# Kernel optimization log

Hardware: AMD Instinct MI355X
Metric: run time of the kernel (lower is better)

## Reference

```python
import jax, jax.numpy as jnp
import numpy as np
import math

E = 1024   # embedding_dim
H = 16     # num_attention_heads
DH = 64    # head_embedding_dim
THD = H * DH
EPS = 1e-5

def _layernorm(x, g, b):
    m = jnp.mean(x, axis=-1, keepdims=True)
    v = jnp.mean(jnp.square(x - m), axis=-1, keepdims=True)
    return (x - m) * jax.lax.rsqrt(v + EPS) * g + b

def setup_inputs() -> dict:
    key = jax.random.key(0)
    ks = jax.random.split(key, 16)
    s_in = 1.0 / math.sqrt(E)
    s_o = 1.0 / math.sqrt(THD)
    inp = {"tokens": jax.random.normal(ks[0], (2, 2048, E), dtype=jnp.float32)}
    # q_linear / k_linear / v_linear: LayerNorm(E) then Linear(E -> THD)
    for i, name in enumerate(["q", "k", "v"]):
        inp[f"ln_{name}_g"] = jnp.ones((E,), jnp.float32)
        inp[f"ln_{name}_b"] = jnp.zeros((E,), jnp.float32)
        inp[f"W{name}"] = jax.random.uniform(ks[1 + 2 * i], (E, THD), jnp.float32, -s_in, s_in)
        inp[f"b{name}"] = jax.random.uniform(ks[2 + 2 * i], (THD,), jnp.float32, -s_in, s_in)
    # attention_linear: LayerNorm(THD) then Linear(THD -> E)
    inp["ln_o_g"] = jnp.ones((THD,), jnp.float32)
    inp["ln_o_b"] = jnp.zeros((THD,), jnp.float32)
    inp["Wo"] = jax.random.uniform(ks[7], (THD, E), jnp.float32, -s_o, s_o)
    inp["bo"] = jax.random.uniform(ks[8], (E,), jnp.float32, -s_o, s_o)
    return inp

def reference(tokens, ln_q_g, ln_q_b, Wq, bq, ln_k_g, ln_k_b, Wk, bk,
              ln_v_g, ln_v_b, Wv, bv, ln_o_g, ln_o_b, Wo, bo):
    N, L, _ = tokens.shape
    # NOTE: faithful to source quirk -- k comes from v_linear, v comes from k_linear.
    q = (_layernorm(tokens, ln_q_g, ln_q_b) @ Wq + bq).reshape(N, L, H, DH).transpose(0, 2, 1, 3)  # (N,H,L,Dh)
    k = (_layernorm(tokens, ln_v_g, ln_v_b) @ Wv + bv).reshape(N, L, H, DH).transpose(0, 2, 3, 1)  # (N,H,Dh,L)
    v = (_layernorm(tokens, ln_k_g, ln_k_b) @ Wk + bk).reshape(N, L, H, DH).transpose(0, 2, 1, 3)  # (N,H,L,Dh)
    qkT = jnp.einsum('bhid,bhdj->bhij', q, k)  # (N,H,L,L)
    # mask added BEFORE dividing by sqrt(Dh), as in source
    mask = jnp.triu(jnp.full((L, L), -9999.0, dtype=qkT.dtype), k=1)
    attn = jax.nn.softmax((qkT + mask) / math.sqrt(DH), axis=-1)
    wv = jnp.einsum('bhij,bhjd->bhid', attn, v).transpose(0, 2, 1, 3).reshape(N, L, THD)
    out = _layernorm(wv, ln_o_g, ln_o_b) @ Wo + bo + tokens
    return (out, k, v)
```

## Files before the change

kernel.cpp:

```cpp
#include <hip/hip_runtime.h>

#define L_SEQ 2048
#define NH    16
#define E_DIM 1024
#define M_ROWS 4096

typedef unsigned short u16;
typedef unsigned int   u32;
typedef __attribute__((ext_vector_type(8))) __bf16 bf16x8;
typedef __attribute__((ext_vector_type(4))) float  f32x4;

__device__ __forceinline__ u16 f2bf(float f) {
  union { float f; u32 u; } x; x.f = f;
  u32 u = x.u;
  return (u16)((u + 0x7FFFu + ((u >> 16) & 1u)) >> 16);
}
__device__ __forceinline__ float bf2f(u16 v) {
  union { u32 u; float f; } x; x.u = ((u32)v) << 16;
  return x.f;
}
__device__ __forceinline__ void st_bf4(u16* p, float a, float b, float c, float d) {
  ushort4 u; u.x = f2bf(a); u.y = f2bf(b); u.z = f2bf(c); u.w = f2bf(d);
  *reinterpret_cast<ushort4*>(p) = u;
}
__device__ __forceinline__ void gload16(const u16* g, u16* l) {
  __builtin_amdgcn_global_load_lds(
      (const __attribute__((address_space(1))) void*)g,
      (__attribute__((address_space(3))) void*)l, 16, 0, 0);
}
#define SBAR() asm volatile("s_barrier" ::: "memory")

__global__ __launch_bounds__(256) void ln_hat_f32(const float* __restrict__ x, u16* __restrict__ o)
{
  __shared__ float red[8];
  const size_t row = blockIdx.x;
  const int t = threadIdx.x;
  float4 v = reinterpret_cast<const float4*>(x + row * E_DIM)[t];
  float s = v.x + v.y + v.z + v.w;
  float q = v.x*v.x + v.y*v.y + v.z*v.z + v.w*v.w;
  #pragma unroll
  for (int off = 32; off; off >>= 1) { s += __shfl_down(s, off); q += __shfl_down(q, off); }
  if ((t & 63) == 0) { red[t >> 6] = s; red[4 + (t >> 6)] = q; }
  __syncthreads();
  float S = red[0] + red[1] + red[2] + red[3];
  float Q = red[4] + red[5] + red[6] + red[7];
  float mean = S * (1.f / E_DIM);
  float rstd = rsqrtf(Q * (1.f / E_DIM) - mean * mean + 1e-5f);
  st_bf4(o + row * E_DIM + t * 4,
         (v.x - mean) * rstd, (v.y - mean) * rstd, (v.z - mean) * rstd, (v.w - mean) * rstd);
}

__global__ __launch_bounds__(256) void ln_hat_bf16(const u16* __restrict__ x, u16* __restrict__ o)
{
  __shared__ float red[8];
  const size_t row = blockIdx.x;
  const int t = threadIdx.x;
  ushort4 u = reinterpret_cast<const ushort4*>(x + row * E_DIM)[t];
  float v0 = bf2f(u.x), v1 = bf2f(u.y), v2 = bf2f(u.z), v3 = bf2f(u.w);
  float s = v0 + v1 + v2 + v3;
  float q = v0*v0 + v1*v1 + v2*v2 + v3*v3;
  #pragma unroll
  for (int off = 32; off; off >>= 1) { s += __shfl_down(s, off); q += __shfl_down(q, off); }
  if ((t & 63) == 0) { red[t >> 6] = s; red[4 + (t >> 6)] = q; }
  __syncthreads();
  float S = red[0] + red[1] + red[2] + red[3];
  float Q = red[4] + red[5] + red[6] + red[7];
  float mean = S * (1.f / E_DIM);
  float rstd = rsqrtf(Q * (1.f / E_DIM) - mean * mean + 1e-5f);
  st_bf4(o + row * E_DIM + t * 4,
         (v0 - mean) * rstd, (v1 - mean) * rstd, (v2 - mean) * rstd, (v3 - mean) * rstd);
}

__global__ __launch_bounds__(256) void transpose_all(
    const float* __restrict__ W0, const float* __restrict__ W1,
    const float* __restrict__ W2, const float* __restrict__ W3,
    const float* __restrict__ g0, const float* __restrict__ g1,
    const float* __restrict__ g2, const float* __restrict__ g3,
    u16* __restrict__ T0, u16* __restrict__ T1, u16* __restrict__ T2, u16* __restrict__ T3)
{
  __shared__ float tile[32][33];
  const int z = blockIdx.z;
  const float* W = (z == 0) ? W0 : (z == 1) ? W1 : (z == 2) ? W2 : W3;
  const float* g = (z == 0) ? g0 : (z == 1) ? g1 : (z == 2) ? g2 : g3;
  u16* T = (z == 0) ? T0 : (z == 1) ? T1 : (z == 2) ? T2 : T3;
  const int tx = threadIdx.x & 31, ty = threadIdx.x >> 5;
  const int bx = blockIdx.x * 32, by = blockIdx.y * 32;
  #pragma unroll
  for (int r = 0; r < 4; ++r) {
    const int e = by + ty + r * 8;
    tile[ty + r * 8][tx] = W[(size_t)e * E_DIM + bx + tx] * g[e];
  }
  __syncthreads();
  #pragma unroll
  for (int r = 0; r < 4; ++r)
    T[(size_t)(bx + ty + r * 8) * E_DIM + by + tx] = f2bf(tile[tx][ty + r * 8]);
}

__global__ __launch_bounds__(256) void bias_fold(
    const float* __restrict__ W0, const float* __restrict__ W1,
    const float* __restrict__ W2, const float* __restrict__ W3,
    const float* __restrict__ l0, const float* __restrict__ l1,
    const float* __restrict__ l2, const float* __restrict__ l3,
    const float* __restrict__ b0, const float* __restrict__ b1,
    const float* __restrict__ b2, const float* __restrict__ b3,
    float* __restrict__ bfold)
{
  __shared__ float part[8][32];
  const int z = blockIdx.y;
  const float* W  = (z == 0) ? W0 : (z == 1) ? W1 : (z == 2) ? W2 : W3;
  const float* bl = (z == 0) ? l0 : (z == 1) ? l1 : (z == 2) ? l2 : l3;
  const float* bs = (z == 0) ? b0 : (z == 1) ? b1 : (z == 2) ? b2 : b3;
  const int tn = threadIdx.x & 31, te = threadIdx.x >> 5;
  const int n = blockIdx.x * 32 + tn;
  float acc = 0.f;
  const int e0 = te * 128;
  for (int e = e0; e < e0 + 128; ++e) acc += bl[e] * W[(size_t)e * E_DIM + n];
  part[te][tn] = acc;
  __syncthreads();
  if (te == 0) {
    float s = part[0][tn] + part[1][tn] + part[2][tn] + part[3][tn]
            + part[4][tn] + part[5][tn] + part[6][tn] + part[7][tn];
    bfold[z * E_DIM + n] = bs[n] + s;
  }
}

#define GBK 64
__device__ __forceinline__ void core128(
    const u16* __restrict__ A, const u16* __restrict__ BT,
    int m0, int n0, int t, u16* lds, f32x4 (&acc)[4][4])
{
  const int lane = t & 63, wave = t >> 6;
  const int wm = wave >> 1, wn = wave & 1;
  const int fr = lane & 15, hi = lane >> 4;
  const int sx = fr & 7;

  auto STAGE = [&](int buf, int kt) {
    u16* la = lds + (buf * 2 + 0) * (128 * GBK);
    u16* lb = lds + (buf * 2 + 1) * (128 * GBK);
    #pragma unroll
    for (int s = 0; s < 4; ++s) {
      const int seg = t + s * 256;
      const int r = seg >> 3;
      const int gc = (seg & 7) ^ (r & 7);
      gload16(A + (size_t)(m0 + r) * E_DIM + kt * GBK + gc * 8, la + seg * 8);
    }
    #pragma unroll
    for (int s = 0; s < 4; ++s) {
      const int seg = t + s * 256;
      const int r = seg >> 3;
      const int gc = (seg & 7) ^ (r & 7);
      gload16(BT + (size_t)(n0 + r) * E_DIM + kt * GBK + gc * 8, lb + seg * 8);
    }
  };
  auto AF = [&](int buf, int i, int ks) -> bf16x8 {
    return *reinterpret_cast<const bf16x8*>(
        lds + (buf * 2 + 0) * (128 * GBK) + (wm * 64 + i * 16 + fr) * GBK + (((ks * 4 + hi) ^ sx) * 8));
  };
  auto BF = [&](int buf, int j, int ks) -> bf16x8 {
    return *reinterpret_cast<const bf16x8*>(
        lds + (buf * 2 + 1) * (128 * GBK) + (wn * 64 + j * 16 + fr) * GBK + (((ks * 4 + hi) ^ sx) * 8));
  };
  auto PHASES = [&](int buf) {
    bf16x8 a[4][2], b[4][2];
    #pragma unroll
    for (int i = 0; i < 4; ++i) { a[i][0] = AF(buf, i, 0); a[i][1] = AF(buf, i, 1); }
    #pragma unroll
    for (int j = 0; j < 4; ++j) { b[j][0] = BF(buf, j, 0); b[j][1] = BF(buf, j, 1); }
    __builtin_amdgcn_s_setprio(1);
    #pragma unroll
    for (int i = 0; i < 4; ++i)
      #pragma unroll
      for (int j = 0; j < 4; ++j) {
        acc[i][j] = __builtin_amdgcn_mfma_f32_16x16x32_bf16(a[i][0], b[j][0], acc[i][j], 0, 0, 0);
        acc[i][j] = __builtin_amdgcn_mfma_f32_16x16x32_bf16(a[i][1], b[j][1], acc[i][j], 0, 0, 0);
      }
    __builtin_amdgcn_s_setprio(0);
  };

  STAGE(0, 0);
  #pragma unroll 1
  for (int kt = 0; kt < 15; ++kt) {
    const int buf = kt & 1;
    SBAR();
    STAGE(buf ^ 1, kt + 1);
    asm volatile("s_waitcnt vmcnt(8)" ::: "memory");
    SBAR();
    PHASES(buf);
  }
  asm volatile("s_waitcnt vmcnt(0)" ::: "memory");
  SBAR();
  PHASES(1);
}

__global__ __launch_bounds__(256, 2) void gemm_qkv128(
    const u16* __restrict__ xhat, const u16* __restrict__ WTcat,
    const float* __restrict__ bfold,
    float* __restrict__ kout, float* __restrict__ vout,
    u16* __restrict__ qbf, u16* __restrict__ kbf, u16* __restrict__ vTb)
{
  __shared__ u16 lds[4 * 128 * GBK];
  const int t = threadIdx.x;
  const int sw = (blockIdx.x & 7) * 96 + (blockIdx.x >> 3);
  const int by = sw / 24, bx = sw % 24;
  const int m0 = by * 128, n0 = bx * 128;

  f32x4 acc[4][4] = {};
  core128(xhat, WTcat, m0, n0, t, lds, acc);

  const int lane = t & 63, wave = t >> 6;
  const int wm = wave >> 1, wn = wave & 1;
  const int fr = lane & 15, hi = lane >> 4;
  const int z = n0 >> 10;
  const float* bias = bfold + z * E_DIM;
  const int rowb = hi * 4;
  #pragma unroll
  for (int i = 0; i < 4; ++i) {
    const int mbase = m0 + wm * 64 + i * 16 + rowb;
    #pragma unroll
    for (int j = 0; j < 4; ++j) {
      const int ng = n0 + wn * 64 + j * 16 + fr;
      const int ncol = ng & 1023;
      const float bval = bias[ncol];
      #pragma unroll
      for (int r = 0; r < 4; ++r) {
        const int m = mbase + r;
        const float val = acc[i][j][r] + bval;
        const int b = m >> 11, l = m & 2047, h = ncol >> 6, d = ncol & 63;
        const size_t bh = (size_t)(b * NH + h);
        if (z == 0) {
          qbf[((bh * L_SEQ + l) << 6) + d] = f2bf(val);
        } else if (z == 1) {
          kout[(bh * 64 + d) * L_SEQ + l] = val;
          kbf[((bh * L_SEQ + l) << 6) + d] = f2bf(val);
        } else {
          vout[(bh * L_SEQ + l) * 64 + d] = val;
          vTb[(bh * 64 + d) * L_SEQ + l] = f2bf(val);
        }
      }
    }
  }
}

__global__ __launch_bounds__(256, 2) void gemm_o128(
    const u16* __restrict__ A, const u16* __restrict__ BT, const float* __restrict__ bias,
    const float* __restrict__ tokens, float* __restrict__ out)
{
  __shared__ u16 lds[4 * 128 * GBK];
  const int t = threadIdx.x;
  const int sw = (blockIdx.x & 7) * 32 + (blockIdx.x >> 3);
  const int by = sw / 8, bx = sw % 8;
  const int m0 = by * 128, n0 = bx * 128;

  f32x4 acc[4][4] = {};
  core128(A, BT, m0, n0, t, lds, acc);

  const int lane = t & 63, wave = t >> 6;
  const int wm = wave >> 1, wn = wave & 1;
  const int fr = lane & 15, hi = lane >> 4;
  const int rowb = hi * 4;
  #pragma unroll
  for (int i = 0; i < 4; ++i) {
    const int mbase = m0 + wm * 64 + i * 16 + rowb;
    #pragma unroll
    for (int j = 0; j < 4; ++j) {
      const int ncol = n0 + wn * 64 + j * 16 + fr;
      const float bval = bias[ncol];
      #pragma unroll
      for (int r = 0; r < 4; ++r) {
        const int m = mbase + r;
        out[(size_t)m * E_DIM + ncol] = acc[i][j][r] + bval + tokens[(size_t)m * E_DIM + ncol];
      }
    }
  }
}

__global__ __launch_bounds__(256) void attn_mfma(
    const u16* __restrict__ qbf, const u16* __restrict__ kbf,
    const u16* __restrict__ vTb, u16* __restrict__ wv)
{
  __shared__ u16 Klds[64][72];
  __shared__ u16 Vlds[64][72];
  __shared__ u16 Plds[4][16][72];
  const int t = threadIdx.x, lane = t & 63, wave = t >> 6;
  const int bi = blockIdx.x;
  const int bh = (bi & 7) + 8 * ((bi >> 3) & 3);
  const int pr = bi >> 5;
  const int fr = lane & 15, hi = lane >> 4;
  const u16* kbase = kbf + (size_t)bh * L_SEQ * 64;
  const u16* vbase = vTb + (size_t)bh * 64 * L_SEQ;
  const int b = bh >> 4, h = bh & 15;

  #pragma unroll 1
  for (int half = 0; half < 2; ++half) {
    const int qt = half ? (31 - pr) : pr;
    const int q0w = qt * 64 + wave * 16;
    const int qg = q0w + fr;

    const u16* qrow = qbf + ((size_t)bh * L_SEQ + q0w + fr) * 64 + hi * 8;
    const bf16x8 qf0 = *reinterpret_cast<const bf16x8*>(qrow);
    const bf16x8 qf1 = *reinterpret_cast<const bf16x8*>(qrow + 32);

    f32x4 o[4] = {};
    float mrun = -3.0e38f, lrun = 0.f;

    for (int tkv = 0; tkv <= qt; ++tkv) {
      const int j0 = tkv * 64;
      const bool diag = (tkv == qt);
      #pragma unroll
      for (int s = 0; s < 2; ++s) {
        const int seg = t + s * 256;
        const int r = seg >> 3, c8 = (seg & 7) * 8;
        *reinterpret_cast<uint4*>(&Klds[r][c8]) =
            *reinterpret_cast<const uint4*>(kbase + (size_t)(j0 + r) * 64 + c8);
        *reinterpret_cast<uint4*>(&Vlds[r][c8]) =
            *reinterpret_cast<const uint4*>(vbase + (size_t)r * L_SEQ + j0 + c8);
      }
      __syncthreads();

      f32x4 st[4] = {};
      __builtin_amdgcn_s_setprio(1);
      #pragma unroll
      for (int kt = 0; kt < 4; ++kt) {
        bf16x8 ka0 = *reinterpret_cast<const bf16x8*>(&Klds[kt*16 + fr][hi*8]);
        bf16x8 ka1 = *reinterpret_cast<const bf16x8*>(&Klds[kt*16 + fr][32 + hi*8]);
        st[kt] = __builtin_amdgcn_mfma_f32_16x16x32_bf16(ka0, qf0, st[kt], 0, 0, 0);
        st[kt] = __builtin_amdgcn_mfma_f32_16x16x32_bf16(ka1, qf1, st[kt], 0, 0, 0);
      }
      __builtin_amdgcn_s_setprio(0);

      float p[16];
      float pmax = -3.0e38f;
      #pragma unroll
      for (int kt = 0; kt < 4; ++kt)
        #pragma unroll
        for (int r = 0; r < 4; ++r) {
          const int key = j0 + kt*16 + hi*4 + r;
          const float v = st[kt][r] * 0.125f +
                          ((diag && key > qg) ? -1249.875f : 0.f);
          p[kt*4 + r] = v;
          pmax = fmaxf(pmax, v);
        }
      pmax = fmaxf(pmax, __shfl_xor(pmax, 16));
      pmax = fmaxf(pmax, __shfl_xor(pmax, 32));
      const float mnew = fmaxf(mrun, pmax);
      const float alpha = __expf(mrun - mnew);
      float lsum = 0.f;
      #pragma unroll
      for (int i = 0; i < 16; ++i) { p[i] = __expf(p[i] - mnew); lsum += p[i]; }
      lsum += __shfl_xor(lsum, 16);
      lsum += __shfl_xor(lsum, 32);
      lrun = lrun * alpha + lsum;
      mrun = mnew;
      #pragma unroll
      for (int r = 0; r < 4; ++r) {
        const float ar = __shfl(alpha, hi*4 + r);
        o[0][r] *= ar; o[1][r] *= ar; o[2][r] *= ar; o[3][r] *= ar;
      }

      #pragma unroll
      for (int kt = 0; kt < 4; ++kt) {
        ushort4 w4;
        w4.x = f2bf(p[kt*4+0]); w4.y = f2bf(p[kt*4+1]);
        w4.z = f2bf(p[kt*4+2]); w4.w = f2bf(p[kt*4+3]);
        *reinterpret_cast<ushort4*>(&Plds[wave][fr][kt*16 + hi*4]) = w4;
      }

      const bf16x8 pf0 = *reinterpret_cast<const bf16x8*>(&Plds[wave][fr][hi*8]);
      const bf16x8 pf1 = *reinterpret_cast<const bf16x8*>(&Plds[wave][fr][32 + hi*8]);
      __builtin_amdgcn_s_setprio(1);
      #pragma unroll
      for (int dt = 0; dt < 4; ++dt) {
        bf16x8 vf0 = *reinterpret_cast<const bf16x8*>(&Vlds[dt*16 + fr][hi*8]);
        bf16x8 vf1 = *reinterpret_cast<const bf16x8*>(&Vlds[dt*16 + fr][32 + hi*8]);
        o[dt] = __builtin_amdgcn_mfma_f32_16x16x32_bf16(pf0, vf0, o[dt], 0, 0, 0);
        o[dt] = __builtin_amdgcn_mfma_f32_16x16x32_bf16(pf1, vf1, o[dt], 0, 0, 0);
      }
      __builtin_amdgcn_s_setprio(0);
      __syncthreads();
    }

    const float inv = 1.f / lrun;
    #pragma unroll
    for (int r = 0; r < 4; ++r) {
      const float ir = __shfl(inv, hi*4 + r);
      const int q = q0w + hi*4 + r;
      u16* dst = wv + (size_t)(b * L_SEQ + q) * E_DIM + h * 64 + fr;
      #pragma unroll
      for (int dt = 0; dt < 4; ++dt)
        dst[dt * 16] = f2bf(o[dt][r] * ir);
    }
  }
}

extern "C" void kernel_launch(void* const* d_in, const int* in_sizes, int n_in,
                              void* d_out, int out_size, void* d_ws, size_t ws_size,
                              hipStream_t stream) {
  (void)in_sizes; (void)n_in; (void)out_size; (void)ws_size;
  const float* tokens = (const float*)d_in[0];
  const float* ln_q_g = (const float*)d_in[1];
  const float* ln_q_b = (const float*)d_in[2];
  const float* Wq     = (const float*)d_in[3];
  const float* bq     = (const float*)d_in[4];
  const float* ln_k_g = (const float*)d_in[5];
  const float* ln_k_b = (const float*)d_in[6];
  const float* Wk     = (const float*)d_in[7];
  const float* bk     = (const float*)d_in[8];
  const float* ln_v_g = (const float*)d_in[9];
  const float* ln_v_b = (const float*)d_in[10];
  const float* Wv     = (const float*)d_in[11];
  const float* bv     = (const float*)d_in[12];
  const float* ln_o_g = (const float*)d_in[13];
  const float* ln_o_b = (const float*)d_in[14];
  const float* Wo     = (const float*)d_in[15];
  const float* bo     = (const float*)d_in[16];

  float* out  = (float*)d_out;
  float* kout = out + 4194304;
  float* vout = kout + 4194304;

  char* w = (char*)d_ws;
  const size_t MB = (size_t)1 << 20;
  u16*   WTq   = (u16*)(w + 0 * MB);
  u16*   WTv   = (u16*)(w + 2 * MB);
  u16*   WTk   = (u16*)(w + 4 * MB);
  u16*   WTo   = (u16*)(w + 6 * MB);
  u16*   xhat  = (u16*)(w + 8 * MB);
  u16*   qbf   = (u16*)(w + 16 * MB);
  u16*   kbf   = (u16*)(w + 24 * MB);
  u16*   vTb   = (u16*)(w + 32 * MB);
  u16*   what  = (u16*)(w + 40 * MB);
  float* bfold = (float*)(w + 48 * MB);
  u16*   wvb   = xhat;

  transpose_all<<<dim3(32, 32, 4), 256, 0, stream>>>(
      Wq, Wv, Wk, Wo, ln_q_g, ln_v_g, ln_k_g, ln_o_g, WTq, WTv, WTk, WTo);
  bias_fold<<<dim3(32, 4), 256, 0, stream>>>(
      Wq, Wv, Wk, Wo, ln_q_b, ln_v_b, ln_k_b, ln_o_b, bq, bv, bk, bo, bfold);
  ln_hat_f32<<<M_ROWS, 256, 0, stream>>>(tokens, xhat);
  gemm_qkv128<<<768, 256, 0, stream>>>(xhat, WTq, bfold, kout, vout, qbf, kbf, vTb);
  attn_mfma<<<512, 256, 0, stream>>>(qbf, kbf, vTb, wvb);
  ln_hat_bf16<<<M_ROWS, 256, 0, stream>>>(wvb, what);
  gemm_o128<<<256, 256, 0, stream>>>(what, WTo, bfold + 3 * E_DIM, tokens, out);
}
```

Before: 142.7 us.

## Shrink GEMM K-tile, double-buffer attention KV, lazy rescale, one q-tile per block

The GEMM core's K-tile drops from 64 to 32 and the XOR swizzle is removed, halving LDS per block so occupancy can rise to 3 blocks per CU. The attention kernel stages K/V for the next tile in registers and double-buffers it in LDS to overlap loads with compute. It also skips rescaling the output when the running max grows by at most 8. Each block now handles one query tile instead of a paired early/late tile, with twice the grid. Removing the swizzle may cause LDS bank conflicts, and the unpaired tiles leave blocks with unequal amounts of causal work.

```diff
diff --git a/kernel.cpp b/kernel.cpp
--- a/kernel.cpp
+++ b/kernel.cpp
@@ -124,7 +124,7 @@
   }
 }
 
-#define GBK 64
+#define GBK 32
 __device__ __forceinline__ void core128(
     const u16* __restrict__ A, const u16* __restrict__ BT,
     int m0, int n0, int t, u16* lds, f32x4 (&acc)[4][4])
@@ -132,58 +132,49 @@
   const int lane = t & 63, wave = t >> 6;
   const int wm = wave >> 1, wn = wave & 1;
   const int fr = lane & 15, hi = lane >> 4;
-  const int sx = fr & 7;
 
   auto STAGE = [&](int buf, int kt) {
     u16* la = lds + (buf * 2 + 0) * (128 * GBK);
     u16* lb = lds + (buf * 2 + 1) * (128 * GBK);
     #pragma unroll
-    for (int s = 0; s < 4; ++s) {
+    for (int s = 0; s < 2; ++s) {
       const int seg = t + s * 256;
-      const int r = seg >> 3;
-      const int gc = (seg & 7) ^ (r & 7);
-      gload16(A + (size_t)(m0 + r) * E_DIM + kt * GBK + gc * 8, la + seg * 8);
-    }
-    #pragma unroll
-    for (int s = 0; s < 4; ++s) {
+      const int r = seg >> 2, c8 = (seg & 3) * 8;
+      gload16(A + (size_t)(m0 + r) * E_DIM + kt * GBK + c8, la + seg * 8);
+    }
+    #pragma unroll
+    for (int s = 0; s < 2; ++s) {
       const int seg = t + s * 256;
-      const int r = seg >> 3;
-      const int gc = (seg & 7) ^ (r & 7);
-      gload16(BT + (size_t)(n0 + r) * E_DIM + kt * GBK + gc * 8, lb + seg * 8);
-    }
-  };
-  auto AF = [&](int buf, int i, int ks) -> bf16x8 {
-    return *reinterpret_cast<const bf16x8*>(
-        lds + (buf * 2 + 0) * (128 * GBK) + (wm * 64 + i * 16 + fr) * GBK + (((ks * 4 + hi) ^ sx) * 8));
-  };
-  auto BF = [&](int buf, int j, int ks) -> bf16x8 {
-    return *reinterpret_cast<const bf16x8*>(
-        lds + (buf * 2 + 1) * (128 * GBK) + (wn * 64 + j * 16 + fr) * GBK + (((ks * 4 + hi) ^ sx) * 8));
+      const int r = seg >> 2, c8 = (seg & 3) * 8;
+      gload16(BT + (size_t)(n0 + r) * E_DIM + kt * GBK + c8, lb + seg * 8);
+    }
   };
   auto PHASES = [&](int buf) {
-    bf16x8 a[4][2], b[4][2];
-    #pragma unroll
-    for (int i = 0; i < 4; ++i) { a[i][0] = AF(buf, i, 0); a[i][1] = AF(buf, i, 1); }
-    #pragma unroll
-    for (int j = 0; j < 4; ++j) { b[j][0] = BF(buf, j, 0); b[j][1] = BF(buf, j, 1); }
+    const u16* la = lds + (buf * 2 + 0) * (128 * GBK);
+    const u16* lb = lds + (buf * 2 + 1) * (128 * GBK);
+    bf16x8 a[4], b[4];
+    #pragma unroll
+    for (int i = 0; i < 4; ++i)
+      a[i] = *reinterpret_cast<const bf16x8*>(&la[(wm * 64 + i * 16 + fr) * GBK + hi * 8]);
+    #pragma unroll
+    for (int j = 0; j < 4; ++j)
+      b[j] = *reinterpret_cast<const bf16x8*>(&lb[(wn * 64 + j * 16 + fr) * GBK + hi * 8]);
     __builtin_amdgcn_s_setprio(1);
     #pragma unroll
     for (int i = 0; i < 4; ++i)
       #pragma unroll
-      for (int j = 0; j < 4; ++j) {
-        acc[i][j] = __builtin_amdgcn_mfma_f32_16x16x32_bf16(a[i][0], b[j][0], acc[i][j], 0, 0, 0);
-        acc[i][j] = __builtin_amdgcn_mfma_f32_16x16x32_bf16(a[i][1], b[j][1], acc[i][j], 0, 0, 0);
-      }
+      for (int j = 0; j < 4; ++j)
+        acc[i][j] = __builtin_amdgcn_mfma_f32_16x16x32_bf16(a[i], b[j], acc[i][j], 0, 0, 0);
     __builtin_amdgcn_s_setprio(0);
   };
 
   STAGE(0, 0);
   #pragma unroll 1
-  for (int kt = 0; kt < 15; ++kt) {
+  for (int kt = 0; kt < 31; ++kt) {
     const int buf = kt & 1;
     SBAR();
     STAGE(buf ^ 1, kt + 1);
-    asm volatile("s_waitcnt vmcnt(8)" ::: "memory");
+    asm volatile("s_waitcnt vmcnt(4)" ::: "memory");
     SBAR();
     PHASES(buf);
   }
@@ -192,7 +183,7 @@
   PHASES(1);
 }
 
-__global__ __launch_bounds__(256, 2) void gemm_qkv128(
+__global__ __launch_bounds__(256, 3) void gemm_qkv128(
     const u16* __restrict__ xhat, const u16* __restrict__ WTcat,
     const float* __restrict__ bfold,
     float* __restrict__ kout, float* __restrict__ vout,
@@ -241,7 +232,7 @@
   }
 }
 
-__global__ __launch_bounds__(256, 2) void gemm_o128(
+__global__ __launch_bounds__(256, 3) void gemm_o128(
     const u16* __restrict__ A, const u16* __restrict__ BT, const float* __restrict__ bias,
     const float* __restrict__ tokens, float* __restrict__ out)
 {
@@ -278,117 +269,130 @@
     const u16* __restrict__ qbf, const u16* __restrict__ kbf,
     const u16* __restrict__ vTb, u16* __restrict__ wv)
 {
-  __shared__ u16 Klds[64][72];
-  __shared__ u16 Vlds[64][72];
+  __shared__ u16 Klds[2][64][72];
+  __shared__ u16 Vlds[2][64][72];
   __shared__ u16 Plds[4][16][72];
   const int t = threadIdx.x, lane = t & 63, wave = t >> 6;
   const int bi = blockIdx.x;
   const int bh = (bi & 7) + 8 * ((bi >> 3) & 3);
-  const int pr = bi >> 5;
+  const int qt = 31 - (bi >> 5);
   const int fr = lane & 15, hi = lane >> 4;
   const u16* kbase = kbf + (size_t)bh * L_SEQ * 64;
   const u16* vbase = vTb + (size_t)bh * 64 * L_SEQ;
   const int b = bh >> 4, h = bh & 15;
 
+  const int q0w = qt * 64 + wave * 16;
+  const int qg = q0w + fr;
+  const u16* qrow = qbf + ((size_t)bh * L_SEQ + q0w + fr) * 64 + hi * 8;
+  const bf16x8 qf0 = *reinterpret_cast<const bf16x8*>(qrow);
+  const bf16x8 qf1 = *reinterpret_cast<const bf16x8*>(qrow + 32);
+
+  f32x4 o[4] = {};
+  float mrun = -3.0e38f, lrun = 0.f;
+
+  uint4 kreg[2], vreg[2];
+  auto LD = [&](int j0) {
+    #pragma unroll
+    for (int s = 0; s < 2; ++s) {
+      const int seg = t + s * 256, r = seg >> 3, c8 = (seg & 7) * 8;
+      kreg[s] = *reinterpret_cast<const uint4*>(kbase + (size_t)(j0 + r) * 64 + c8);
+      vreg[s] = *reinterpret_cast<const uint4*>(vbase + (size_t)r * L_SEQ + j0 + c8);
+    }
+  };
+  auto ST = [&](int buf) {
+    #pragma unroll
+    for (int s = 0; s < 2; ++s) {
+      const int seg = t + s * 256, r = seg >> 3, c8 = (seg & 7) * 8;
+      *reinterpret_cast<uint4*>(&Klds[buf][r][c8]) = kreg[s];
+      *reinterpret_cast<uint4*>(&Vlds[buf][r][c8]) = vreg[s];
+    }
+  };
+
+  LD(0); ST(0);
+  __syncthreads();
   #pragma unroll 1
-  for (int half = 0; half < 2; ++half) {
-    const int qt = half ? (31 - pr) : pr;
-    const int q0w = qt * 64 + wave * 16;
-    const int qg = q0w + fr;
-
-    const u16* qrow = qbf + ((size_t)bh * L_SEQ + q0w + fr) * 64 + hi * 8;
-    const bf16x8 qf0 = *reinterpret_cast<const bf16x8*>(qrow);
-    const bf16x8 qf1 = *reinterpret_cast<const bf16x8*>(qrow + 32);
-
-    f32x4 o[4] = {};
-    float mrun = -3.0e38f, lrun = 0.f;
-
-    for (int tkv = 0; tkv <= qt; ++tkv) {
-      const int j0 = tkv * 64;
-      const bool diag = (tkv == qt);
+  for (int tkv = 0; tkv <= qt; ++tkv) {
+    const int buf = tkv & 1;
+    const int j0 = tkv * 64;
+    const bool diag = (tkv == qt);
+    if (tkv < qt) LD(j0 + 64);
+
+    f32x4 st[4] = {};
+    __builtin_amdgcn_s_setprio(1);
+    #pragma unroll
+    for (int kt = 0; kt < 4; ++kt) {
+      bf16x8 ka0 = *reinterpret_cast<const bf16x8*>(&Klds[buf][kt*16 + fr][hi*8]);
+      bf16x8 ka1 = *reinterpret_cast<const bf16x8*>(&Klds[buf][kt*16 + fr][32 + hi*8]);
+      st[kt] = __builtin_amdgcn_mfma_f32_16x16x32_bf16(ka0, qf0, st[kt], 0, 0, 0);
+      st[kt] = __builtin_amdgcn_mfma_f32_16x16x32_bf16(ka1, qf1, st[kt], 0, 0, 0);
+    }
+    __builtin_amdgcn_s_setprio(0);
+
+    float p[16];
+    float pmax = -3.0e38f;
+    #pragma unroll
+    for (int kt = 0; kt < 4; ++kt)
       #pragma unroll
-      for (int s = 0; s < 2; ++s) {
-        const int seg = t + s * 256;
-        const int r = seg >> 3, c8 = (seg & 7) * 8;
-        *reinterpret_cast<uint4*>(&Klds[r][c8]) =
-            *reinterpret_cast<const uint4*>(kbase + (size_t)(j0 + r) * 64 + c8);
-        *reinterpret_cast<uint4*>(&Vlds[r][c8]) =
-            *reinterpret_cast<const uint4*>(vbase + (size_t)r * L_SEQ + j0 + c8);
+      for (int r = 0; r < 4; ++r) {
+        const int key = j0 + kt*16 + hi*4 + r;
+        const float v = st[kt][r] * 0.125f +
+                        ((diag && key > qg) ? -1249.875f : 0.f);
+        p[kt*4 + r] = v;
+        pmax = fmaxf(pmax, v);
       }
-      __syncthreads();
-
-      f32x4 st[4] = {};
-      __builtin_amdgcn_s_setprio(1);
-      #pragma unroll
-      for (int kt = 0; kt < 4; ++kt) {
-        bf16x8 ka0 = *reinterpret_cast<const bf16x8*>(&Klds[kt*16 + fr][hi*8]);
-        bf16x8 ka1 = *reinterpret_cast<const bf16x8*>(&Klds[kt*16 + fr][32 + hi*8]);
-        st[kt] = __builtin_amdgcn_mfma_f32_16x16x32_bf16(ka0, qf0, st[kt], 0, 0, 0);
-        st[kt] = __builtin_amdgcn_mfma_f32_16x16x32_bf16(ka1, qf1, st[kt], 0, 0, 0);
-      }
-      __builtin_amdgcn_s_setprio(0);
-
-      float p[16];
-      float pmax = -3.0e38f;
-      #pragma unroll
-      for (int kt = 0; kt < 4; ++kt)
-        #pragma unroll
-        for (int r = 0; r < 4; ++r) {
-          const int key = j0 + kt*16 + hi*4 + r;
-          const float v = st[kt][r] * 0.125f +
-                          ((diag && key > qg) ? -1249.875f : 0.f);
-          p[kt*4 + r] = v;
-          pmax = fmaxf(pmax, v);
-        }
-      pmax = fmaxf(pmax, __shfl_xor(pmax, 16));
-      pmax = fmaxf(pmax, __shfl_xor(pmax, 32));
+    pmax = fmaxf(pmax, __shfl_xor(pmax, 16));
+    pmax = fmaxf(pmax, __shfl_xor(pmax, 32));
+    if (!__all(pmax - mrun <= 8.f)) {
       const float mnew = fmaxf(mrun, pmax);
       const float alpha = __expf(mrun - mnew);
-      float lsum = 0.f;
-      #pragma unroll
-      for (int i = 0; i < 16; ++i) { p[i] = __expf(p[i] - mnew); lsum += p[i]; }
-      lsum += __shfl_xor(lsum, 16);
-      lsum += __shfl_xor(lsum, 32);
-      lrun = lrun * alpha + lsum;
-      mrun = mnew;
       #pragma unroll
       for (int r = 0; r < 4; ++r) {
         const float ar = __shfl(alpha, hi*4 + r);
         o[0][r] *= ar; o[1][r] *= ar; o[2][r] *= ar; o[3][r] *= ar;
       }
-
-      #pragma unroll
-      for (int kt = 0; kt < 4; ++kt) {
-        ushort4 w4;
-        w4.x = f2bf(p[kt*4+0]); w4.y = f2bf(p[kt*4+1]);
-        w4.z = f2bf(p[kt*4+2]); w4.w = f2bf(p[kt*4+3]);
-        *reinterpret_cast<ushort4*>(&Plds[wave][fr][kt*16 + hi*4]) = w4;
-      }
-
-      const bf16x8 pf0 = *reinterpret_cast<const bf16x8*>(&Plds[wave][fr][hi*8]);
-      const bf16x8 pf1 = *reinterpret_cast<const bf16x8*>(&Plds[wave][fr][32 + hi*8]);
-      __builtin_amdgcn_s_setprio(1);
-      #pragma unroll
-      for (int dt = 0; dt < 4; ++dt) {
-        bf16x8 vf0 = *reinterpret_cast<const bf16x8*>(&Vlds[dt*16 + fr][hi*8]);
-        bf16x8 vf1 = *reinterpret_cast<const bf16x8*>(&Vlds[dt*16 + fr][32 + hi*8]);
-        o[dt] = __builtin_amdgcn_mfma_f32_16x16x32_bf16(pf0, vf0, o[dt], 0, 0, 0);
-        o[dt] = __builtin_amdgcn_mfma_f32_16x16x32_bf16(pf1, vf1, o[dt], 0, 0, 0);
-      }
-      __builtin_amdgcn_s_setprio(0);
-      __syncthreads();
-    }
-
-    const float inv = 1.f / lrun;
-    #pragma unroll
-    for (int r = 0; r < 4; ++r) {
-      const float ir = __shfl(inv, hi*4 + r);
-      const int q = q0w + hi*4 + r;
-      u16* dst = wv + (size_t)(b * L_SEQ + q) * E_DIM + h * 64 + fr;
-      #pragma unroll
-      for (int dt = 0; dt < 4; ++dt)
-        dst[dt * 16] = f2bf(o[dt][r] * ir);
-    }
+      lrun *= alpha;
+      mrun = mnew;
+    }
+    float lsum = 0.f;
+    #pragma unroll
+    for (int i = 0; i < 16; ++i) { p[i] = __expf(p[i] - mrun); lsum += p[i]; }
+    lsum += __shfl_xor(lsum, 16);
+    lsum += __shfl_xor(lsum, 32);
+    lrun += lsum;
+
+    #pragma unroll
+    for (int kt = 0; kt < 4; ++kt) {
+      ushort4 w4;
+      w4.x = f2bf(p[kt*4+0]); w4.y = f2bf(p[kt*4+1]);
+      w4.z = f2bf(p[kt*4+2]); w4.w = f2bf(p[kt*4+3]);
+      *reinterpret_cast<ushort4*>(&Plds[wave][fr][kt*16 + hi*4]) = w4;
+    }
+
+    const bf16x8 pf0 = *reinterpret_cast<const bf16x8*>(&Plds[wave][fr][hi*8]);
+    const bf16x8 pf1 = *reinterpret_cast<const bf16x8*>(&Plds[wave][fr][32 + hi*8]);
+    __builtin_amdgcn_s_setprio(1);
+    #pragma unroll
+    for (int dt = 0; dt < 4; ++dt) {
+      bf16x8 vf0 = *reinterpret_cast<const bf16x8*>(&Vlds[buf][dt*16 + fr][hi*8]);
+      bf16x8 vf1 = *reinterpret_cast<const bf16x8*>(&Vlds[buf][dt*16 + fr][32 + hi*8]);
+      o[dt] = __builtin_amdgcn_mfma_f32_16x16x32_bf16(pf0, vf0, o[dt], 0, 0, 0);
+      o[dt] = __builtin_amdgcn_mfma_f32_16x16x32_bf16(pf1, vf1, o[dt], 0, 0, 0);
+    }
+    __builtin_amdgcn_s_setprio(0);
+
+    if (tkv < qt) ST(buf ^ 1);
+    __syncthreads();
+  }
+
+  const float inv = 1.f / lrun;
+  #pragma unroll
+  for (int r = 0; r < 4; ++r) {
+    const float ir = __shfl(inv, hi*4 + r);
+    const int q = q0w + hi*4 + r;
+    u16* dst = wv + (size_t)(b * L_SEQ + q) * E_DIM + h * 64 + fr;
+    #pragma unroll
+    for (int dt = 0; dt < 4; ++dt)
+      dst[dt * 16] = f2bf(o[dt][r] * ir);
   }
 }
 
@@ -438,7 +442,7 @@
       Wq, Wv, Wk, Wo, ln_q_b, ln_v_b, ln_k_b, ln_o_b, bq, bv, bk, bo, bfold);
   ln_hat_f32<<<M_ROWS, 256, 0, stream>>>(tokens, xhat);
   gemm_qkv128<<<768, 256, 0, stream>>>(xhat, WTq, bfold, kout, vout, qbf, kbf, vTb);
-  attn_mfma<<<512, 256, 0, stream>>>(qbf, kbf, vTb, wvb);
+  attn_mfma<<<1024, 256, 0, stream>>>(qbf, kbf, vTb, wvb);
   ln_hat_bf16<<<M_ROWS, 256, 0, stream>>>(wvb, what);
   gemm_o128<<<256, 256, 0, stream>>>(what, WTo, bfold + 3 * E_DIM, tokens, out);
 }
```

New measurement: 176.2 us. 1.23x slower.

## Remap GEMM tiles per XCD, use exp2 softmax and packed bf16 conversion

Applied to the files above, without the earlier changes.

Changes the block-to-tile mapping of the QKV and output GEMMs so that each XCD works on a contiguous 2D patch of tiles, which should improve L2 reuse of A and B panels. In attention, the softmax scale is folded with log2(e) so exp2f can replace __expf, and the mask constant is rescaled to match. P is converted to bf16 with the packed hip_bf16 intrinsic instead of manual per-element rounding. These are independent tweaks, and the mask constant is a rounded approximation of -1249.875·log2e.

```diff
diff --git a/kernel.cpp b/kernel.cpp
--- a/kernel.cpp
+++ b/kernel.cpp
@@ -1,4 +1,5 @@
 #include <hip/hip_runtime.h>
+#include <hip/hip_bf16.h>
 
 #define L_SEQ 2048
 #define NH    16
@@ -22,6 +23,10 @@
 __device__ __forceinline__ void st_bf4(u16* p, float a, float b, float c, float d) {
   ushort4 u; u.x = f2bf(a); u.y = f2bf(b); u.z = f2bf(c); u.w = f2bf(d);
   *reinterpret_cast<ushort4*>(p) = u;
+}
+__device__ __forceinline__ u32 pkbf(float a, float b) {
+  __hip_bfloat162 h = __float22bfloat162_rn(float2{a, b});
+  return *reinterpret_cast<u32*>(&h);
 }
 __device__ __forceinline__ void gload16(const u16* g, u16* l) {
   __builtin_amdgcn_global_load_lds(
@@ -200,8 +205,9 @@
 {
   __shared__ u16 lds[4 * 128 * GBK];
   const int t = threadIdx.x;
-  const int sw = (blockIdx.x & 7) * 96 + (blockIdx.x >> 3);
-  const int by = sw / 24, bx = sw % 24;
+  const int xcd = blockIdx.x & 7, l = blockIdx.x >> 3;
+  const int by = 8 * (xcd >> 1) + l / 12;
+  const int bx = 12 * (xcd & 1) + l % 12;
   const int m0 = by * 128, n0 = bx * 128;
 
   f32x4 acc[4][4] = {};
@@ -225,16 +231,16 @@
       for (int r = 0; r < 4; ++r) {
         const int m = mbase + r;
         const float val = acc[i][j][r] + bval;
-        const int b = m >> 11, l = m & 2047, h = ncol >> 6, d = ncol & 63;
+        const int b = m >> 11, ltok = m & 2047, h = ncol >> 6, d = ncol & 63;
         const size_t bh = (size_t)(b * NH + h);
         if (z == 0) {
-          qbf[((bh * L_SEQ + l) << 6) + d] = f2bf(val);
+          qbf[((bh * L_SEQ + ltok) << 6) + d] = f2bf(val);
         } else if (z == 1) {
-          kout[(bh * 64 + d) * L_SEQ + l] = val;
-          kbf[((bh * L_SEQ + l) << 6) + d] = f2bf(val);
+          kout[(bh * 64 + d) * L_SEQ + ltok] = val;
+          kbf[((bh * L_SEQ + ltok) << 6) + d] = f2bf(val);
         } else {
-          vout[(bh * L_SEQ + l) * 64 + d] = val;
-          vTb[(bh * 64 + d) * L_SEQ + l] = f2bf(val);
+          vout[(bh * L_SEQ + ltok) * 64 + d] = val;
+          vTb[(bh * 64 + d) * L_SEQ + ltok] = f2bf(val);
         }
       }
     }
@@ -247,8 +253,9 @@
 {
   __shared__ u16 lds[4 * 128 * GBK];
   const int t = threadIdx.x;
-  const int sw = (blockIdx.x & 7) * 32 + (blockIdx.x >> 3);
-  const int by = sw / 8, bx = sw % 8;
+  const int xcd = blockIdx.x & 7, l = blockIdx.x >> 3;
+  const int by = 8 * (xcd >> 1) + (l >> 2);
+  const int bx = 4 * (xcd & 1) + (l & 3);
   const int m0 = by * 128, n0 = bx * 128;
 
   f32x4 acc[4][4] = {};
@@ -289,6 +296,8 @@
   const u16* kbase = kbf + (size_t)bh * L_SEQ * 64;
   const u16* vbase = vTb + (size_t)bh * 64 * L_SEQ;
   const int b = bh >> 4, h = bh & 15;
+  const float kSC2  = 0.125f * 1.44269504089f;
+  const float kMSK2 = -1803.2f;
 
   #pragma unroll 1
   for (int half = 0; half < 2; ++half) {
@@ -335,18 +344,17 @@
         #pragma unroll
         for (int r = 0; r < 4; ++r) {
           const int key = j0 + kt*16 + hi*4 + r;
-          const float v = st[kt][r] * 0.125f +
-                          ((diag && key > qg) ? -1249.875f : 0.f);
+          const float v = st[kt][r] * kSC2 + ((diag && key > qg) ? kMSK2 : 0.f);
           p[kt*4 + r] = v;
           pmax = fmaxf(pmax, v);
         }
       pmax = fmaxf(pmax, __shfl_xor(pmax, 16));
       pmax = fmaxf(pmax, __shfl_xor(pmax, 32));
       const float mnew = fmaxf(mrun, pmax);
-      const float alpha = __expf(mrun - mnew);
+      const float alpha = exp2f(mrun - mnew);
       float lsum = 0.f;
       #pragma unroll
-      for (int i = 0; i < 16; ++i) { p[i] = __expf(p[i] - mnew); lsum += p[i]; }
+      for (int i = 0; i < 16; ++i) { p[i] = exp2f(p[i] - mnew); lsum += p[i]; }
       lsum += __shfl_xor(lsum, 16);
       lsum += __shfl_xor(lsum, 32);
       lrun = lrun * alpha + lsum;
@@ -359,10 +367,10 @@
 
       #pragma unroll
       for (int kt = 0; kt < 4; ++kt) {
-        ushort4 w4;
-        w4.x = f2bf(p[kt*4+0]); w4.y = f2bf(p[kt*4+1]);
-        w4.z = f2bf(p[kt*4+2]); w4.w = f2bf(p[kt*4+3]);
-        *reinterpret_cast<ushort4*>(&Plds[wave][fr][kt*16 + hi*4]) = w4;
+        uint2 w2;
+        w2.x = pkbf(p[kt*4+0], p[kt*4+1]);
+        w2.y = pkbf(p[kt*4+2], p[kt*4+3]);
+        *reinterpret_cast<uint2*>(&Plds[wave][fr][kt*16 + hi*4]) = w2;
       }
 
       const bf16x8 pf0 = *reinterpret_cast<const bf16x8*>(&Plds[wave][fr][hi*8]);
```

Result: no change. 142.4 us (-0.2%).
